# Kernel tuning notes

Measured on AMD Instinct MI355X. Metric: run time of the kernel, lower is better.

Reference implementation:

```python
import jax, jax.numpy as jnp
import numpy as np

T, B, N, F = 128, 8, 32, 128
H = 256  # hidden channels
DEG = 8


def setup_inputs() -> dict:
    key = jax.random.key(0)
    ks = jax.random.split(key, 8)
    data = jax.random.normal(ks[0], (T, B, N, F), jnp.float32)
    all_ohs = jax.random.normal(ks[1], (T, B, N, 8), jnp.float32)
    n0 = B * N * T
    n1 = B * N * (T // 2)
    edge_index0 = jax.random.randint(ks[2], (2, n0 * DEG), 0, n0)
    edge_index1 = jax.random.randint(ks[3], (2, n1 * DEG), 0, n1)
    def init(k, shape, fan):
        return jax.random.normal(k, shape, jnp.float32) / np.float32(np.sqrt(fan))
    W0 = init(ks[4], (2 * F, H), 2 * F); b0 = jnp.zeros((H,), jnp.float32)
    Wc0 = init(ks[5], (H, H, 5), H * 5); bc0 = jnp.zeros((H,), jnp.float32)
    W1 = init(ks[6], (2 * H, H), 2 * H); b1 = jnp.zeros((H,), jnp.float32)
    Wc1 = init(ks[7], (H, H, 5), H * 5); bc1 = jnp.zeros((H,), jnp.float32)
    return dict(data=data, all_ohs=all_ohs,
                edge_index0=edge_index0, edge_index1=edge_index1,
                W0=W0, b0=b0, Wc0=Wc0, bc0=bc0,
                W1=W1, b1=b1, Wc1=Wc1, bc1=bc1)


def edge_conv(x, edge_index, W, b):
    # PyG EdgeConv: out_i = max_{(j->i)} relu(Linear(cat[x_i, x_j - x_i]))
    src, dst = edge_index[0], edge_index[1]
    x_i = x[dst]           # [E, C] target features
    x_j = x[src]           # [E, C] source features
    msg = jax.nn.relu(jnp.concatenate([x_i, x_j - x_i], axis=-1) @ W + b)
    out = jax.ops.segment_max(msg, dst, num_segments=x.shape[0])
    return jnp.where(jnp.isneginf(out), 0.0, out)  # empty segments -> 0 (PyG fill)


def temp_conv(x, Wc, bc):
    # x: [BN, C, L]; Conv1d(k=5, pad=2) + relu + MaxPool1d(2)
    y = jax.lax.conv_general_dilated(x, Wc, (1,), [(2, 2)],
                                     dimension_numbers=('NCH', 'OIH', 'NCH'))
    y = jax.nn.relu(y + bc[None, :, None])
    L2 = y.shape[-1] // 2
    y = y[..., : L2 * 2].reshape(y.shape[0], y.shape[1], L2, 2)
    return jnp.max(y, axis=-1)


def reference(data, all_ohs, edge_index0, edge_index1,
              W0, b0, Wc0, bc0, W1, b1, Wc1, bc1):
    # 'fast' path, context=False: all_ohs unused beyond reshape
    length = data.shape[0]
    x = data.reshape(T, B * N, F).transpose(1, 0, 2).reshape(-1, F)  # [BN*T, F]
    layers = ((edge_index0, W0, b0, Wc0, bc0),
              (edge_index1, W1, b1, Wc1, bc1))
    for ei, W, b, Wc, bc in layers:
        x = edge_conv(x, ei, W, b)                       # [BN*length, C]
        x = x.reshape(-1, length, x.shape[-1])           # [BN, length, C]
        x = x.transpose(0, 2, 1)                         # [BN, C, length]
        x = temp_conv(x, Wc, bc)                         # [BN, C, length//2]
        length = x.shape[2]
        C = x.shape[1]
        x = x.transpose(0, 2, 1).reshape(-1, C)          # [BN*length, C]
    return x
```

## Files before the change

### kernel.cpp

```cpp
#include <hip/hip_runtime.h>
#include <hip/hip_bf16.h>
#include <math.h>

#define T0 128
#define BN 256
#define Ff 128
#define Hh 256
#define NODE0 32768
#define E0 262144
#define T1 64
#define NODE1 16384
#define E1 131072
#define CAP 48

typedef __attribute__((ext_vector_type(8))) short bhalf8;
typedef __attribute__((ext_vector_type(4))) float floatx4;
typedef __attribute__((ext_vector_type(16))) float floatx16;

__device__ __forceinline__ unsigned short f2bf(float x) {
  union { float f; unsigned u; } v; v.f = x;
  unsigned r = v.u + 0x7fff + ((v.u >> 16) & 1);
  return (unsigned short)(r >> 16);
}
__device__ __forceinline__ float bf2f(unsigned short b) {
  union { unsigned u; float f; } v; v.u = ((unsigned)b) << 16;
  return v.f;
}

__global__ void k_prepfill(const float* __restrict__ data, unsigned short* __restrict__ X0b,
                           const float* __restrict__ W0, unsigned short* __restrict__ Wbot0,
                           unsigned short* __restrict__ Wd0,
                           const float* __restrict__ W1, unsigned short* __restrict__ Wbot1,
                           unsigned short* __restrict__ Wd1,
                           const float* __restrict__ Wc0, unsigned short* __restrict__ Wtb0,
                           const float* __restrict__ Wc1, unsigned short* __restrict__ Wtb1,
                           const int* __restrict__ ei0, const int* __restrict__ ei1,
                           int* __restrict__ cnt0, int* __restrict__ cnt1,
                           int* __restrict__ slot0, int* __restrict__ slot1) {
  int b = blockIdx.x;
  int tid = threadIdx.x;
  if (b < 2048) {
    int idx = b * 256 + tid;
    int c8 = idx & 15;
    int r  = idx >> 4;
    int t  = r & (T0 - 1);
    int bn = r >> 7;
    const float* s = data + ((size_t)t * BN + bn) * Ff + c8 * 8;
    float4 a = *(const float4*)s;
    float4 bb = *(const float4*)(s + 4);
    unsigned short o[8];
    o[0] = f2bf(a.x); o[1] = f2bf(a.y); o[2] = f2bf(a.z); o[3] = f2bf(a.w);
    o[4] = f2bf(bb.x); o[5] = f2bf(bb.y); o[6] = f2bf(bb.z); o[7] = f2bf(bb.w);
    *(int4*)(X0b + ((size_t)(bn * T0 + t) * Ff + c8 * 8)) = *(int4*)o;
  } else if (b < 2176) {
    int idx = (b - 2048) * 256 + tid;
    int n = idx >> 7, k = idx & 127;
    float top = W0[(size_t)k * 256 + n];
    float bot = W0[(size_t)(128 + k) * 256 + n];
    Wbot0[idx] = f2bf(bot);
    Wd0[idx]   = f2bf(top - bot);
  } else if (b < 2432) {
    int idx = (b - 2176) * 256 + tid;
    int n = idx >> 8, k = idx & 255;
    float top = W1[(size_t)k * 256 + n];
    float bot = W1[(size_t)(256 + k) * 256 + n];
    Wbot1[idx] = f2bf(bot);
    Wd1[idx]   = f2bf(top - bot);
  } else if (b < 3712) {
    int idx = (b - 2432) * 256 + tid;
    int tap = idx >> 16, o = (idx >> 8) & 255, i = idx & 255;
    Wtb0[idx] = f2bf(Wc0[((size_t)o * 256 + i) * 5 + tap]);
  } else if (b < 4992) {
    int idx = (b - 3712) * 256 + tid;
    int tap = idx >> 16, o = (idx >> 8) & 255, i = idx & 255;
    Wtb1[idx] = f2bf(Wc1[((size_t)o * 256 + i) * 5 + tap]);
  } else {
    int e = (b - 4992) * 256 + tid;
    if (e < E0) {
      int d = ei0[E0 + e];
      int p = atomicAdd(&cnt0[d], 1);
      if (p < CAP) slot0[(size_t)d * CAP + p] = ei0[e];
    } else {
      int e2 = e - E0;
      int d = ei1[E1 + e2];
      int p = atomicAdd(&cnt1[d], 1);
      if (p < CAP) slot1[(size_t)d * CAP + p] = ei1[e2];
    }
  }
}

__global__ __launch_bounds__(256) void k_gemm2(const unsigned short* __restrict__ A,
                                               const unsigned short* __restrict__ Wbot,
                                               const unsigned short* __restrict__ Wd,
                                               unsigned short* __restrict__ Bm,
                                               unsigned short* __restrict__ P, int K,
                                               const float* __restrict__ bias) {
  __shared__ __align__(16) short A_lds[64 * 72];
  __shared__ __align__(16) short B0_lds[128 * 72];
  __shared__ __align__(16) short B1_lds[128 * 72];
  int tid = threadIdx.x;
  int row0 = blockIdx.x * 64;
  int col0 = blockIdx.y * 128;
  int lane = tid & 63, wv = tid >> 6;
  int m16 = lane & 15, quad = lane >> 4;
  int sr = tid >> 3, sseg = tid & 7;

  floatx4 accB[8], accP[8];
#pragma unroll
  for (int nt = 0; nt < 8; ++nt) {
    accB[nt] = (floatx4){0.f, 0.f, 0.f, 0.f};
    accP[nt] = (floatx4){0.f, 0.f, 0.f, 0.f};
  }

  for (int kb = 0; kb < K; kb += 64) {
    __syncthreads();
#pragma unroll
    for (int i = 0; i < 2; ++i) {
      int r = sr + i * 32;
      *(int4*)&A_lds[r * 72 + sseg * 8] =
          *(const int4*)(A + (size_t)(row0 + r) * K + kb + sseg * 8);
    }
#pragma unroll
    for (int i = 0; i < 4; ++i) {
      int r = sr + i * 32;
      *(int4*)&B0_lds[r * 72 + sseg * 8] =
          *(const int4*)(Wbot + (size_t)(col0 + r) * K + kb + sseg * 8);
      *(int4*)&B1_lds[r * 72 + sseg * 8] =
          *(const int4*)(Wd + (size_t)(col0 + r) * K + kb + sseg * 8);
    }
    __syncthreads();
#pragma unroll
    for (int ks = 0; ks < 2; ++ks) {
      bhalf8 a = *(const bhalf8*)&A_lds[(wv * 16 + m16) * 72 + ks * 32 + quad * 8];
#pragma unroll
      for (int nt = 0; nt < 8; ++nt) {
        bhalf8 b0 = *(const bhalf8*)&B0_lds[(nt * 16 + m16) * 72 + ks * 32 + quad * 8];
        accB[nt] = __builtin_amdgcn_mfma_f32_16x16x32_bf16(a, b0, accB[nt], 0, 0, 0);
        bhalf8 b1 = *(const bhalf8*)&B1_lds[(nt * 16 + m16) * 72 + ks * 32 + quad * 8];
        accP[nt] = __builtin_amdgcn_mfma_f32_16x16x32_bf16(a, b1, accP[nt], 0, 0, 0);
      }
    }
  }

  int g0 = row0 + wv * 16 + quad * 4;
#pragma unroll
  for (int nt = 0; nt < 8; ++nt) {
    int c = col0 + nt * 16 + m16;
    float bv = bias[c];
#pragma unroll
    for (int r = 0; r < 4; ++r) {
      Bm[(size_t)(g0 + r) * 256 + c] = f2bf(accB[nt][r]);
      P[(size_t)(g0 + r) * 256 + c]  = f2bf(accP[nt][r] + bv);
    }
  }
}

__global__ __launch_bounds__(256) void k_maxg2(const unsigned short* __restrict__ Bm,
                                               const int* __restrict__ cnt,
                                               const int* __restrict__ slot,
                                               const unsigned short* __restrict__ P,
                                               unsigned short* __restrict__ X1) {
  int node = blockIdx.x * 4 + (threadIdx.x >> 6);
  int lane = threadIdx.x & 63;
  int n = cnt[node];
  if (n > CAP) n = CAP;
  const int* sl = slot + (size_t)node * CAP;
  float4 m = make_float4(-INFINITY, -INFINITY, -INFINITY, -INFINITY);
  for (int i = 0; i < n; i += 8) {
    int s[8];
#pragma unroll
    for (int j = 0; j < 8; ++j) {
      int idx = i + j;
      s[j] = sl[(idx < n) ? idx : (n - 1)];
    }
    ushort4 v[8];
#pragma unroll
    for (int j = 0; j < 8; ++j)
      v[j] = *(const ushort4*)(Bm + (size_t)s[j] * 256 + lane * 4);
#pragma unroll
    for (int j = 0; j < 8; ++j) {
      m.x = fmaxf(m.x, bf2f(v[j].x));
      m.y = fmaxf(m.y, bf2f(v[j].y));
      m.z = fmaxf(m.z, bf2f(v[j].z));
      m.w = fmaxf(m.w, bf2f(v[j].w));
    }
  }
  ushort4 p = *(const ushort4*)(P + (size_t)node * 256 + lane * 4);
  ushort4 o;
  o.x = f2bf(fmaxf(bf2f(p.x) + m.x, 0.f));
  o.y = f2bf(fmaxf(bf2f(p.y) + m.y, 0.f));
  o.z = f2bf(fmaxf(bf2f(p.z) + m.z, 0.f));
  o.w = f2bf(fmaxf(bf2f(p.w) + m.w, 0.f));
  *(ushort4*)(X1 + (size_t)node * 256 + lane * 4) = o;
}

template <int TRows, int NT, bool OUT_F32>
__global__ __launch_bounds__(256) void k_conv32(const unsigned short* __restrict__ X,
                                                const unsigned short* __restrict__ Wtb,
                                                const float* __restrict__ bc,
                                                void* __restrict__ Yout) {
  const int CB = NT * 64;
  __shared__ __align__(16) short A_lds[2 * 68 * 40];
  __shared__ __align__(16) short B_lds[5 * CB * 40];
  int tid = threadIdx.x;
  int row0 = blockIdx.x * 128;
  int col0 = blockIdx.y * CB;
  int lane = tid & 63, wv = tid >> 6;
  int l31 = lane & 31, khalf = lane >> 5;
  int h = wv & 1, cpart = wv >> 1;

  floatx16 acc[2][NT];
#pragma unroll
  for (int rt = 0; rt < 2; ++rt)
#pragma unroll
    for (int ct = 0; ct < NT; ++ct)
#pragma unroll
      for (int r = 0; r < 16; ++r) acc[rt][ct][r] = 0.f;

  for (int kb = 0; kb < 256; kb += 32) {
    __syncthreads();
    for (int u = tid; u < 544; u += 256) {
      int s = (u >= 272) ? 1 : 0;
      int v = u - s * 272;
      int rr = v >> 2, seg = v & 3;
      int base = row0 + s * 64;
      int lo = base & ~(TRows - 1);
      int gr = base + rr - 2;
      int4 val = {0, 0, 0, 0};
      if (gr >= lo && gr < lo + TRows)
        val = *(const int4*)(X + (size_t)gr * 256 + kb + seg * 8);
      *(int4*)&A_lds[(s * 68 + rr) * 40 + seg * 8] = val;
    }
#pragma unroll
    for (int i = 0; i < 5 * NT; ++i) {
      int u = tid + i * 256;
      int r = u >> 2, seg = u & 3;
      int tap = r / CB, col = r % CB;
      *(int4*)&B_lds[r * 40 + seg * 8] =
          *(const int4*)(Wtb + (size_t)tap * 65536 + (size_t)(col0 + col) * 256 + kb + seg * 8);
    }
    __syncthreads();
#pragma unroll
    for (int tap = 0; tap < 5; ++tap) {
#pragma unroll
      for (int ks = 0; ks < 2; ++ks) {
        int ko = ks * 16 + khalf * 8;
        bhalf8 a[2];
#pragma unroll
        for (int rt = 0; rt < 2; ++rt)
          a[rt] = *(const bhalf8*)&A_lds[(h * 68 + rt * 32 + l31 + tap) * 40 + ko];
#pragma unroll
        for (int ct = 0; ct < NT; ++ct) {
          bhalf8 b = *(const bhalf8*)&B_lds[(tap * CB + cpart * NT * 32 + ct * 32 + l31) * 40 + ko];
#pragma unroll
          for (int rt = 0; rt < 2; ++rt)
            acc[rt][ct] = __builtin_amdgcn_mfma_f32_32x32x16_bf16(a[rt], b, acc[rt][ct], 0, 0, 0);
        }
      }
    }
  }

#pragma unroll
  for (int rt = 0; rt < 2; ++rt) {
#pragma unroll
    for (int ct = 0; ct < NT; ++ct) {
      int c = col0 + cpart * NT * 32 + ct * 32 + l31;
      float bv = bc[c];
#pragma unroll
      for (int r = 0; r < 16; r += 2) {
        int rowg = row0 + h * 64 + rt * 32 + 4 * khalf + 8 * (r >> 2) + (r & 3);
        float y0 = fmaxf(acc[rt][ct][r] + bv, 0.f);
        float y1 = fmaxf(acc[rt][ct][r + 1] + bv, 0.f);
        float p = fmaxf(y0, y1);
        int o = rowg >> 1;
        if (OUT_F32) ((float*)Yout)[(size_t)o * 256 + c] = p;
        else ((unsigned short*)Yout)[(size_t)o * 256 + c] = f2bf(p);
      }
    }
  }
}

extern "C" void kernel_launch(void* const* d_in, const int* in_sizes, int n_in,
                              void* d_out, int out_size, void* d_ws, size_t ws_size,
                              hipStream_t stream) {
  const float* data = (const float*)d_in[0];
  const int* ei0 = (const int*)d_in[2];
  const int* ei1 = (const int*)d_in[3];
  const float* W0  = (const float*)d_in[4];
  const float* b0  = (const float*)d_in[5];
  const float* Wc0 = (const float*)d_in[6];
  const float* bc0 = (const float*)d_in[7];
  const float* W1  = (const float*)d_in[8];
  const float* b1  = (const float*)d_in[9];
  const float* Wc1 = (const float*)d_in[10];
  const float* bc1 = (const float*)d_in[11];
  float* out = (float*)d_out;

  char* base = (char*)d_ws;
  size_t off = 0;
  auto alloc = [&](size_t bytes) { void* p = base + off; off += (bytes + 255) & ~(size_t)255; return p; };
  unsigned short* X0b   = (unsigned short*)alloc((size_t)NODE0 * Ff * 2);
  unsigned short* Bm    = (unsigned short*)alloc((size_t)NODE0 * Hh * 2);
  unsigned short* P     = (unsigned short*)alloc((size_t)NODE0 * Hh * 2);
  unsigned short* X1b   = (unsigned short*)alloc((size_t)NODE0 * Hh * 2);
  unsigned short* Y0b   = (unsigned short*)alloc((size_t)NODE1 * Hh * 2);
  unsigned short* Wbot0 = (unsigned short*)alloc(256 * 128 * 2);
  unsigned short* Wd0   = (unsigned short*)alloc(256 * 128 * 2);
  unsigned short* Wbot1 = (unsigned short*)alloc(256 * 256 * 2);
  unsigned short* Wd1   = (unsigned short*)alloc(256 * 256 * 2);
  unsigned short* Wtb0  = (unsigned short*)alloc(5 * 65536 * 2);
  unsigned short* Wtb1  = (unsigned short*)alloc(5 * 65536 * 2);
  int* cnt0  = (int*)alloc(NODE0 * 4);
  int* cnt1  = (int*)alloc(NODE1 * 4);
  int* slot0 = (int*)alloc((size_t)NODE0 * CAP * 4);
  int* slot1 = (int*)alloc((size_t)NODE1 * CAP * 4);

  hipMemsetAsync(cnt0, 0, (NODE0 + NODE1) * sizeof(int), stream);

  k_prepfill<<<6528, 256, 0, stream>>>(data, X0b, W0, Wbot0, Wd0, W1, Wbot1, Wd1,
                                       Wc0, Wtb0, Wc1, Wtb1,
                                       ei0, ei1, cnt0, cnt1, slot0, slot1);

  k_gemm2<<<dim3(NODE0 / 64, 2), 256, 0, stream>>>(X0b, Wbot0, Wd0, Bm, P, 128, b0);
  k_maxg2<<<NODE0 / 4, 256, 0, stream>>>(Bm, cnt0, slot0, P, X1b);
  k_conv32<128, 1, false><<<dim3(NODE0 / 128, 4), 256, 0, stream>>>(X1b, Wtb0, bc0, Y0b);

  k_gemm2<<<dim3(NODE1 / 64, 2), 256, 0, stream>>>(Y0b, Wbot1, Wd1, Bm, P, 256, b1);
  k_maxg2<<<NODE1 / 4, 256, 0, stream>>>(Bm, cnt1, slot1, P, X1b);
  k_conv32<64, 1, true><<<dim3(NODE1 / 128, 4), 256, 0, stream>>>(X1b, Wtb1, bc1, out);
}
```

Before: 213.1 us.

## Fuse input transpose/bf16 cast into first GEMM and retile temporal conv

The fp32-to-bf16 transpose of the input data is removed from the prep kernel. It is now done inside the first edge GEMM's A-tile load, which drops the X0b intermediate buffer and a full write and read of it. The temporal conv kernel is also retiled to 256 rows by 64 columns per block, with each wave owning a 64-row window and a 2x2 set of 32x32 MFMA tiles. This halves the grid and reuses each loaded B tile across more rows, at the cost of uncoalesced strided fp32 loads in the GEMM and more LDS per conv block.

```diff
diff --git a/kernel.cpp b/kernel.cpp
--- a/kernel.cpp
+++ b/kernel.cpp
@@ -27,8 +27,7 @@
   return v.f;
 }
 
-__global__ void k_prepfill(const float* __restrict__ data, unsigned short* __restrict__ X0b,
-                           const float* __restrict__ W0, unsigned short* __restrict__ Wbot0,
+__global__ void k_prepfill(const float* __restrict__ W0, unsigned short* __restrict__ Wbot0,
                            unsigned short* __restrict__ Wd0,
                            const float* __restrict__ W1, unsigned short* __restrict__ Wbot1,
                            unsigned short* __restrict__ Wd1,
@@ -39,43 +38,30 @@
                            int* __restrict__ slot0, int* __restrict__ slot1) {
   int b = blockIdx.x;
   int tid = threadIdx.x;
-  if (b < 2048) {
+  if (b < 128) {
     int idx = b * 256 + tid;
-    int c8 = idx & 15;
-    int r  = idx >> 4;
-    int t  = r & (T0 - 1);
-    int bn = r >> 7;
-    const float* s = data + ((size_t)t * BN + bn) * Ff + c8 * 8;
-    float4 a = *(const float4*)s;
-    float4 bb = *(const float4*)(s + 4);
-    unsigned short o[8];
-    o[0] = f2bf(a.x); o[1] = f2bf(a.y); o[2] = f2bf(a.z); o[3] = f2bf(a.w);
-    o[4] = f2bf(bb.x); o[5] = f2bf(bb.y); o[6] = f2bf(bb.z); o[7] = f2bf(bb.w);
-    *(int4*)(X0b + ((size_t)(bn * T0 + t) * Ff + c8 * 8)) = *(int4*)o;
-  } else if (b < 2176) {
-    int idx = (b - 2048) * 256 + tid;
     int n = idx >> 7, k = idx & 127;
     float top = W0[(size_t)k * 256 + n];
     float bot = W0[(size_t)(128 + k) * 256 + n];
     Wbot0[idx] = f2bf(bot);
     Wd0[idx]   = f2bf(top - bot);
-  } else if (b < 2432) {
-    int idx = (b - 2176) * 256 + tid;
+  } else if (b < 384) {
+    int idx = (b - 128) * 256 + tid;
     int n = idx >> 8, k = idx & 255;
     float top = W1[(size_t)k * 256 + n];
     float bot = W1[(size_t)(256 + k) * 256 + n];
     Wbot1[idx] = f2bf(bot);
     Wd1[idx]   = f2bf(top - bot);
-  } else if (b < 3712) {
-    int idx = (b - 2432) * 256 + tid;
+  } else if (b < 1664) {
+    int idx = (b - 384) * 256 + tid;
     int tap = idx >> 16, o = (idx >> 8) & 255, i = idx & 255;
     Wtb0[idx] = f2bf(Wc0[((size_t)o * 256 + i) * 5 + tap]);
-  } else if (b < 4992) {
-    int idx = (b - 3712) * 256 + tid;
+  } else if (b < 2944) {
+    int idx = (b - 1664) * 256 + tid;
     int tap = idx >> 16, o = (idx >> 8) & 255, i = idx & 255;
     Wtb1[idx] = f2bf(Wc1[((size_t)o * 256 + i) * 5 + tap]);
   } else {
-    int e = (b - 4992) * 256 + tid;
+    int e = (b - 2944) * 256 + tid;
     if (e < E0) {
       int d = ei0[E0 + e];
       int p = atomicAdd(&cnt0[d], 1);
@@ -89,7 +75,9 @@
   }
 }
 
-__global__ __launch_bounds__(256) void k_gemm2(const unsigned short* __restrict__ A,
+template <bool F32A>
+__global__ __launch_bounds__(256) void k_gemm2(const float* __restrict__ Af,
+                                               const unsigned short* __restrict__ Ab,
                                                const unsigned short* __restrict__ Wbot,
                                                const unsigned short* __restrict__ Wd,
                                                unsigned short* __restrict__ Bm,
@@ -117,8 +105,20 @@
 #pragma unroll
     for (int i = 0; i < 2; ++i) {
       int r = sr + i * 32;
-      *(int4*)&A_lds[r * 72 + sseg * 8] =
-          *(const int4*)(A + (size_t)(row0 + r) * K + kb + sseg * 8);
+      if (F32A) {
+        int rg = row0 + r;
+        int t = rg & (T0 - 1), bn = rg >> 7;
+        const float* s = Af + ((size_t)t * BN + bn) * Ff + kb + sseg * 8;
+        float4 f0 = *(const float4*)s;
+        float4 f1 = *(const float4*)(s + 4);
+        unsigned short o[8];
+        o[0] = f2bf(f0.x); o[1] = f2bf(f0.y); o[2] = f2bf(f0.z); o[3] = f2bf(f0.w);
+        o[4] = f2bf(f1.x); o[5] = f2bf(f1.y); o[6] = f2bf(f1.z); o[7] = f2bf(f1.w);
+        *(int4*)&A_lds[r * 72 + sseg * 8] = *(int4*)o;
+      } else {
+        *(int4*)&A_lds[r * 72 + sseg * 8] =
+            *(const int4*)(Ab + (size_t)(row0 + r) * K + kb + sseg * 8);
+      }
     }
 #pragma unroll
     for (int i = 0; i < 4; ++i) {
@@ -194,48 +194,46 @@
   *(ushort4*)(X1 + (size_t)node * 256 + lane * 4) = o;
 }
 
-template <int TRows, int NT, bool OUT_F32>
+template <int TRows, bool OUT_F32>
 __global__ __launch_bounds__(256) void k_conv32(const unsigned short* __restrict__ X,
                                                 const unsigned short* __restrict__ Wtb,
                                                 const float* __restrict__ bc,
                                                 void* __restrict__ Yout) {
-  const int CB = NT * 64;
-  __shared__ __align__(16) short A_lds[2 * 68 * 40];
-  __shared__ __align__(16) short B_lds[5 * CB * 40];
+  __shared__ __align__(16) short A_lds[4 * 68 * 40];
+  __shared__ __align__(16) short B_lds[5 * 64 * 40];
   int tid = threadIdx.x;
-  int row0 = blockIdx.x * 128;
-  int col0 = blockIdx.y * CB;
+  int row0 = blockIdx.x * 256;
+  int col0 = blockIdx.y * 64;
   int lane = tid & 63, wv = tid >> 6;
   int l31 = lane & 31, khalf = lane >> 5;
-  int h = wv & 1, cpart = wv >> 1;
-
-  floatx16 acc[2][NT];
+
+  floatx16 acc[2][2];
 #pragma unroll
   for (int rt = 0; rt < 2; ++rt)
 #pragma unroll
-    for (int ct = 0; ct < NT; ++ct)
+    for (int ct = 0; ct < 2; ++ct)
 #pragma unroll
       for (int r = 0; r < 16; ++r) acc[rt][ct][r] = 0.f;
 
   for (int kb = 0; kb < 256; kb += 32) {
     __syncthreads();
-    for (int u = tid; u < 544; u += 256) {
-      int s = (u >= 272) ? 1 : 0;
-      int v = u - s * 272;
+    for (int u = tid; u < 1088; u += 256) {
+      int win = u / 272;
+      int v = u - win * 272;
       int rr = v >> 2, seg = v & 3;
-      int base = row0 + s * 64;
+      int base = row0 + win * 64;
       int lo = base & ~(TRows - 1);
       int gr = base + rr - 2;
       int4 val = {0, 0, 0, 0};
       if (gr >= lo && gr < lo + TRows)
         val = *(const int4*)(X + (size_t)gr * 256 + kb + seg * 8);
-      *(int4*)&A_lds[(s * 68 + rr) * 40 + seg * 8] = val;
-    }
-#pragma unroll
-    for (int i = 0; i < 5 * NT; ++i) {
+      *(int4*)&A_lds[(win * 68 + rr) * 40 + seg * 8] = val;
+    }
+#pragma unroll
+    for (int i = 0; i < 5; ++i) {
       int u = tid + i * 256;
       int r = u >> 2, seg = u & 3;
-      int tap = r / CB, col = r % CB;
+      int tap = r >> 6, col = r & 63;
       *(int4*)&B_lds[r * 40 + seg * 8] =
           *(const int4*)(Wtb + (size_t)tap * 65536 + (size_t)(col0 + col) * 256 + kb + seg * 8);
     }
@@ -245,17 +243,14 @@
 #pragma unroll
       for (int ks = 0; ks < 2; ++ks) {
         int ko = ks * 16 + khalf * 8;
-        bhalf8 a[2];
-#pragma unroll
-        for (int rt = 0; rt < 2; ++rt)
-          a[rt] = *(const bhalf8*)&A_lds[(h * 68 + rt * 32 + l31 + tap) * 40 + ko];
-#pragma unroll
-        for (int ct = 0; ct < NT; ++ct) {
-          bhalf8 b = *(const bhalf8*)&B_lds[(tap * CB + cpart * NT * 32 + ct * 32 + l31) * 40 + ko];
-#pragma unroll
-          for (int rt = 0; rt < 2; ++rt)
-            acc[rt][ct] = __builtin_amdgcn_mfma_f32_32x32x16_bf16(a[rt], b, acc[rt][ct], 0, 0, 0);
-        }
+        bhalf8 a0 = *(const bhalf8*)&A_lds[(wv * 68 + l31 + tap) * 40 + ko];
+        bhalf8 a1 = *(const bhalf8*)&A_lds[(wv * 68 + 32 + l31 + tap) * 40 + ko];
+        bhalf8 b0 = *(const bhalf8*)&B_lds[((tap << 6) + l31) * 40 + ko];
+        bhalf8 b1 = *(const bhalf8*)&B_lds[((tap << 6) + 32 + l31) * 40 + ko];
+        acc[0][0] = __builtin_amdgcn_mfma_f32_32x32x16_bf16(a0, b0, acc[0][0], 0, 0, 0);
+        acc[0][1] = __builtin_amdgcn_mfma_f32_32x32x16_bf16(a0, b1, acc[0][1], 0, 0, 0);
+        acc[1][0] = __builtin_amdgcn_mfma_f32_32x32x16_bf16(a1, b0, acc[1][0], 0, 0, 0);
+        acc[1][1] = __builtin_amdgcn_mfma_f32_32x32x16_bf16(a1, b1, acc[1][1], 0, 0, 0);
       }
     }
   }
@@ -263,12 +258,12 @@
 #pragma unroll
   for (int rt = 0; rt < 2; ++rt) {
 #pragma unroll
-    for (int ct = 0; ct < NT; ++ct) {
-      int c = col0 + cpart * NT * 32 + ct * 32 + l31;
+    for (int ct = 0; ct < 2; ++ct) {
+      int c = col0 + ct * 32 + l31;
       float bv = bc[c];
 #pragma unroll
       for (int r = 0; r < 16; r += 2) {
-        int rowg = row0 + h * 64 + rt * 32 + 4 * khalf + 8 * (r >> 2) + (r & 3);
+        int rowg = row0 + wv * 64 + rt * 32 + 4 * khalf + 8 * (r >> 2) + (r & 3);
         float y0 = fmaxf(acc[rt][ct][r] + bv, 0.f);
         float y1 = fmaxf(acc[rt][ct][r + 1] + bv, 0.f);
         float p = fmaxf(y0, y1);
@@ -299,7 +294,6 @@
   char* base = (char*)d_ws;
   size_t off = 0;
   auto alloc = [&](size_t bytes) { void* p = base + off; off += (bytes + 255) & ~(size_t)255; return p; };
-  unsigned short* X0b   = (unsigned short*)alloc((size_t)NODE0 * Ff * 2);
   unsigned short* Bm    = (unsigned short*)alloc((size_t)NODE0 * Hh * 2);
   unsigned short* P     = (unsigned short*)alloc((size_t)NODE0 * Hh * 2);
   unsigned short* X1b   = (unsigned short*)alloc((size_t)NODE0 * Hh * 2);
@@ -317,15 +311,15 @@
 
   hipMemsetAsync(cnt0, 0, (NODE0 + NODE1) * sizeof(int), stream);
 
-  k_prepfill<<<6528, 256, 0, stream>>>(data, X0b, W0, Wbot0, Wd0, W1, Wbot1, Wd1,
+  k_prepfill<<<4480, 256, 0, stream>>>(W0, Wbot0, Wd0, W1, Wbot1, Wd1,
                                        Wc0, Wtb0, Wc1, Wtb1,
                                        ei0, ei1, cnt0, cnt1, slot0, slot1);
 
-  k_gemm2<<<dim3(NODE0 / 64, 2), 256, 0, stream>>>(X0b, Wbot0, Wd0, Bm, P, 128, b0);
+  k_gemm2<true><<<dim3(NODE0 / 64, 2), 256, 0, stream>>>(data, nullptr, Wbot0, Wd0, Bm, P, 128, b0);
   k_maxg2<<<NODE0 / 4, 256, 0, stream>>>(Bm, cnt0, slot0, P, X1b);
-  k_conv32<128, 1, false><<<dim3(NODE0 / 128, 4), 256, 0, stream>>>(X1b, Wtb0, bc0, Y0b);
-
-  k_gemm2<<<dim3(NODE1 / 64, 2), 256, 0, stream>>>(Y0b, Wbot1, Wd1, Bm, P, 256, b1);
+  k_conv32<128, false><<<dim3(NODE0 / 256, 4), 256, 0, stream>>>(X1b, Wtb0, bc0, Y0b);
+
+  k_gemm2<false><<<dim3(NODE1 / 64, 2), 256, 0, stream>>>(nullptr, Y0b, Wbot1, Wd1, Bm, P, 256, b1);
   k_maxg2<<<NODE1 / 4, 256, 0, stream>>>(Bm, cnt1, slot1, P, X1b);
-  k_conv32<64, 1, true><<<dim3(NODE1 / 128, 4), 256, 0, stream>>>(X1b, Wtb1, bc1, out);
-}
+  k_conv32<64, true><<<dim3(NODE1 / 256, 4), 256, 0, stream>>>(X1b, Wtb1, bc1, out);
+}
```

Result: no change. 214.9 us (+0.8%).
